# Kernel optimization log

Measured on AMD Instinct MI355X. Metric: run time of the kernel, lower is better.

Reference implementation:

```python
import jax, jax.numpy as jnp
import numpy as np

EPS = 1e-12  # torch F.normalize default eps


def conv1x1(x, w, b):
    # x: [N,C,H,W], w: [O,C], b: [O]
    return jnp.einsum('nchw,oc->nohw', x, w) + b[None, :, None, None]


def forward_sa(f1, f2, cw1, cb1, cw2, cb2):
    c1 = conv1x1(f1, cw1, cb1)  # [N,1,H,W]
    c2 = conv1x1(f2, cw2, cb2)
    n, _, h, w = c1.shape
    c1 = jax.nn.softmax(c1.reshape(n, 1, h * w), axis=-1).reshape(n, 1, h, w)
    c2 = jax.nn.softmax(c2.reshape(n, 1, h * w), axis=-1).reshape(n, 1, h, w)
    return c1 * f1, c2 * f2


def l2_normalize_ch(x):
    # F.normalize(x): L2 over channel dim (dim=1), norm clamped to eps
    n = jnp.sqrt(jnp.sum(x * x, axis=1, keepdims=True))
    return x / jnp.maximum(n, EPS)


def forward_ca(f1, f2, pw1, pb1, pw2, pb2):
    N, C, H, W = f1.shape
    HW = H * W
    f1_cl = conv1x1(f1, pw1, pb1).reshape(N, -1, HW)  # [N,Cl,HW]
    f2_cl = conv1x1(f2, pw2, pb2).reshape(N, -1, HW)
    # A = f2_cl^T @ f1_cl : [N,HW,HW]
    A_c = jnp.tanh(jnp.einsum('nci,ncj->nij', f2_cl, f1_cl))
    f1_v = f1.reshape(N, C, HW)
    f2_v = f2.reshape(N, C, HW)
    # f1_hat = f1_v @ A_c^T ; f2_hat = f2_v @ A_c
    f1_hat = jnp.einsum('ncj,nij->nci', f1_v, A_c).reshape(N, C, H, W)
    f2_hat = jnp.einsum('ncj,nji->nci', f2_v, A_c).reshape(N, C, H, W)
    return l2_normalize_ch(f1_hat), l2_normalize_ch(f2_hat)


def setup_inputs() -> dict:
    key = jax.random.key(0)
    ks = jax.random.split(key, 10)
    N, C, H, W = 8, 256, 32, 32
    Cl = C // 16
    return {
        'f1': jax.random.normal(ks[0], (N, C, H, W), jnp.float32),
        'f2': jax.random.normal(ks[1], (N, C, H, W), jnp.float32),
        'pw1': jax.random.normal(ks[2], (Cl, C), jnp.float32) * 0.05,
        'pb1': jax.random.normal(ks[3], (Cl,), jnp.float32) * 0.05,
        'pw2': jax.random.normal(ks[4], (Cl, C), jnp.float32) * 0.05,
        'pb2': jax.random.normal(ks[5], (Cl,), jnp.float32) * 0.05,
        'cw1': jax.random.normal(ks[6], (1, C), jnp.float32) * 0.05,
        'cb1': jax.random.normal(ks[7], (1,), jnp.float32) * 0.05,
        'cw2': jax.random.normal(ks[8], (1, C), jnp.float32) * 0.05,
        'cb2': jax.random.normal(ks[9], (1,), jnp.float32) * 0.05,
    }


def reference(f1, f2, pw1, pb1, pw2, pb2, cw1, cb1, cw2, cb2):
    fp1, fp2 = f1, f2
    for i in range(5):
        s1, s2 = forward_sa(fp1, fp2, cw1, cb1, cw2, cb2)
        h1, h2 = forward_ca(s1, s2, pw1, pb1, pw2, pb2)
        if i < 4:
            fp1 = jax.nn.relu(h1 + fp1)
            fp2 = jax.nn.relu(h2 + fp2)
    return h1, h2, s1, s2
```

## Files before the change

### kernel.cpp

```cpp
#include <hip/hip_runtime.h>
#include <cstdint>
#include <cstddef>

#define N_  8
#define C_  256
#define HW_ 1024
#define CL_ 16
#define SZ_ (N_*C_*HW_)
#define WSCALE_ 4096.0f

typedef __attribute__((ext_vector_type(8))) _Float16 half8;
typedef __attribute__((ext_vector_type(4))) float f32x4;

static __device__ __forceinline__ float tanh_fast(float x){
  x = fminf(fmaxf(x, -15.f), 15.f);
  float e = __expf(2.f * x);
  return (e - 1.f) / (e + 1.f);
}

static __device__ __forceinline__ unsigned short f2h(float x){
  _Float16 h = (_Float16)x;
  return *(unsigned short*)&h;
}

static __device__ __forceinline__ void combine16(
    const float* __restrict__ mpart, const float* __restrict__ spart,
    int base, float& m, float& rl)
{
  m = -1e30f;
  #pragma unroll
  for (int k = 0; k < 16; ++k) m = fmaxf(m, mpart[base * 16 + k]);
  float s = 0.f;
  #pragma unroll
  for (int k = 0; k < 16; ++k) s += spart[base * 16 + k] * __expf(mpart[base * 16 + k] - m);
  rl = 1.f / s;
}

#define GLD16(g, l) __builtin_amdgcn_global_load_lds( \
    (const __attribute__((address_space(1))) void*)(g), \
    (__attribute__((address_space(3))) void*)(l), 16, 0, 0)

__global__ __launch_bounds__(256) void k_cvt(
    const float* __restrict__ f1, const float* __restrict__ f2,
    _Float16* __restrict__ o1, _Float16* __restrict__ o2)
{
  const int side = blockIdx.y;
  const size_t o = ((size_t)blockIdx.x * 256 + threadIdx.x) * 8;
  const float* __restrict__ f = side ? f2 : f1;
  _Float16* __restrict__ oo = side ? o2 : o1;
  const float4 v0 = *(const float4*)&f[o];
  const float4 v1 = *(const float4*)&f[o + 4];
  half8 r;
  r[0] = (_Float16)v0.x; r[1] = (_Float16)v0.y; r[2] = (_Float16)v0.z; r[3] = (_Float16)v0.w;
  r[4] = (_Float16)v1.x; r[5] = (_Float16)v1.y; r[6] = (_Float16)v1.z; r[7] = (_Float16)v1.w;
  *(half8*)&oo[o] = r;
}

__global__ __launch_bounds__(256) void k_sa_dot(
    const float* __restrict__ fp1, const float* __restrict__ fp2,
    const float* __restrict__ cw1, const float* __restrict__ cw2,
    const float* __restrict__ pw1, const float* __restrict__ pw2,
    float* __restrict__ cval, float* __restrict__ pdot,
    float* __restrict__ mpart, float* __restrict__ spart)
{
  const int n = blockIdx.z, side = blockIdx.y, hw0 = blockIdx.x * 64;
  const int t = threadIdx.x, hwl = t & 63, cg = t >> 6;
  const float* __restrict__ pw = side ? pw2 : pw1;
  const float* __restrict__ cw = side ? cw2 : cw1;
  const float* __restrict__ f  = (side ? fp2 : fp1) + (size_t)n * C_ * HW_ + hw0 + hwl;
  const int cb = __builtin_amdgcn_readfirstlane(cg * 64);

  float acc[17];
  #pragma unroll
  for (int l = 0; l < 17; ++l) acc[l] = 0.f;

  for (int cc = 0; cc < 64; ++cc){
    const int c = cb + cc;
    const float v = f[(size_t)c * HW_];
    acc[16] += v * cw[c];
    #pragma unroll
    for (int l = 0; l < 16; ++l) acc[l] += v * pw[l * C_ + c];
  }

  __shared__ float red[17][4][64];
  #pragma unroll
  for (int l = 0; l < 17; ++l) red[l][cg][hwl] = acc[l];
  __syncthreads();

  if (t < 64){
    const int base = n * 2 + side;
    float xc = 0.f;
    #pragma unroll
    for (int l = 0; l < 17; ++l){
      const float s = red[l][0][t] + red[l][1][t] + red[l][2][t] + red[l][3][t];
      if (l < 16) pdot[((size_t)base * CL_ + l) * HW_ + hw0 + t] = s;
      else      { cval[(size_t)base * HW_ + hw0 + t] = s; xc = s; }
    }
    float mb = xc;
    #pragma unroll
    for (int off = 32; off; off >>= 1) mb = fmaxf(mb, __shfl_xor(mb, off));
    float e = __expf(xc - mb);
    #pragma unroll
    for (int off = 32; off; off >>= 1) e += __shfl_xor(e, off);
    if (t == 0){
      mpart[base * 16 + blockIdx.x] = mb;
      spart[base * 16 + blockIdx.x] = e;
    }
  }
}

__global__ __launch_bounds__(256) void k_corr(
    const float* __restrict__ cval, const float* __restrict__ pdot,
    const float* __restrict__ pb1, const float* __restrict__ pb2,
    const float* __restrict__ mpart, const float* __restrict__ spart,
    unsigned short* __restrict__ Abf, unsigned short* __restrict__ Atbf)
{
  const int n = blockIdx.z, i0 = blockIdx.y * 64, j0 = blockIdx.x * 64;
  const int b1 = n * 2, b2 = n * 2 + 1;
  __align__(16) __shared__ float s2[CL_][64];
  __align__(16) __shared__ float s1[CL_][64];
  __shared__ unsigned short at_s[64][68];
  const int t = threadIdx.x;
  const int lr = t >> 4, lc = (t & 15) * 4;

  float m1, rl1, m2, rl2;
  combine16(mpart, spart, b1, m1, rl1);
  combine16(mpart, spart, b2, m2, rl2);

  {
    const float bias2 = pb2[lr];
    const float4 c2 = *(const float4*)&cval[(size_t)b2 * HW_ + i0 + lc];
    const float4 p2 = *(const float4*)&pdot[((size_t)b2 * CL_ + lr) * HW_ + i0 + lc];
    s2[lr][lc + 0] = __expf(c2.x - m2) * rl2 * p2.x + bias2;
    s2[lr][lc + 1] = __expf(c2.y - m2) * rl2 * p2.y + bias2;
    s2[lr][lc + 2] = __expf(c2.z - m2) * rl2 * p2.z + bias2;
    s2[lr][lc + 3] = __expf(c2.w - m2) * rl2 * p2.w + bias2;

    const float bias1 = pb1[lr];
    const float4 c1 = *(const float4*)&cval[(size_t)b1 * HW_ + j0 + lc];
    const float4 p1 = *(const float4*)&pdot[((size_t)b1 * CL_ + lr) * HW_ + j0 + lc];
    s1[lr][lc + 0] = __expf(c1.x - m1) * rl1 * p1.x + bias1;
    s1[lr][lc + 1] = __expf(c1.y - m1) * rl1 * p1.y + bias1;
    s1[lr][lc + 2] = __expf(c1.z - m1) * rl1 * p1.z + bias1;
    s1[lr][lc + 3] = __expf(c1.w - m1) * rl1 * p1.w + bias1;
  }
  __syncthreads();

  const int ti = t >> 4, tj = t & 15;
  float acc[4][4];
  #pragma unroll
  for (int a = 0; a < 4; ++a)
    #pragma unroll
    for (int b = 0; b < 4; ++b) acc[a][b] = 0.f;

  #pragma unroll
  for (int l = 0; l < CL_; ++l){
    const float4 a4 = *(const float4*)&s2[l][ti * 4];
    const float4 b4 = *(const float4*)&s1[l][tj * 4];
    const float av[4] = {a4.x, a4.y, a4.z, a4.w};
    const float bv[4] = {b4.x, b4.y, b4.z, b4.w};
    #pragma unroll
    for (int a = 0; a < 4; ++a)
      #pragma unroll
      for (int b = 0; b < 4; ++b) acc[a][b] += av[a] * bv[b];
  }

  float tf[4][4];
  #pragma unroll
  for (int a = 0; a < 4; ++a)
    #pragma unroll
    for (int b = 0; b < 4; ++b) tf[a][b] = tanh_fast(acc[a][b]);

  float w1j[4], w2i[4];
  #pragma unroll
  for (int b = 0; b < 4; ++b)
    w1j[b] = WSCALE_ * __expf(cval[(size_t)b1 * HW_ + j0 + tj * 4 + b] - m1) * rl1;
  #pragma unroll
  for (int a = 0; a < 4; ++a)
    w2i[a] = WSCALE_ * __expf(cval[(size_t)b2 * HW_ + i0 + ti * 4 + a] - m2) * rl2;

  unsigned short* __restrict__ An  = Abf  + ((size_t)n << 20);
  unsigned short* __restrict__ Atn = Atbf + ((size_t)n << 20);
  #pragma unroll
  for (int a = 0; a < 4; ++a){
    ushort4 va;
    va.x = f2h(tf[a][0] * w1j[0]); va.y = f2h(tf[a][1] * w1j[1]);
    va.z = f2h(tf[a][2] * w1j[2]); va.w = f2h(tf[a][3] * w1j[3]);
    *(ushort4*)&An[(size_t)(i0 + ti * 4 + a) * HW_ + j0 + tj * 4] = va;
  }
  #pragma unroll
  for (int b = 0; b < 4; ++b){
    ushort4 vb;
    vb.x = f2h(tf[0][b] * w2i[0]); vb.y = f2h(tf[1][b] * w2i[1]);
    vb.z = f2h(tf[2][b] * w2i[2]); vb.w = f2h(tf[3][b] * w2i[3]);
    *(ushort4*)&at_s[tj * 4 + b][ti * 4] = vb;
  }
  __syncthreads();
  #pragma unroll
  for (int rep = 0; rep < 2; ++rep){
    const int idx = t + rep * 256;
    const int r = idx >> 3, q = (idx & 7) * 8;
    const ushort4 lo = *(const ushort4*)&at_s[r][q];
    const ushort4 hi = *(const ushort4*)&at_s[r][q + 4];
    *(ushort4*)&Atn[(size_t)(j0 + r) * HW_ + i0 + q] = lo;
    *(ushort4*)&Atn[(size_t)(j0 + r) * HW_ + i0 + q + 4] = hi;
  }
}

__global__ __launch_bounds__(512, 2) void k_gemm_fused(
    const _Float16* __restrict__ fhc1, const _Float16* __restrict__ fhc2,
    const unsigned short* __restrict__ Abf, const unsigned short* __restrict__ Atbf,
    const float* __restrict__ fpin1, const float* __restrict__ fpin2,
    float* __restrict__ fpo1, float* __restrict__ fpo2,
    _Float16* __restrict__ fhn1, _Float16* __restrict__ fhn2,
    const float* __restrict__ pw1, const float* __restrict__ pw2,
    const float* __restrict__ cw1, const float* __restrict__ cw2,
    float* __restrict__ cval, float* __restrict__ pdot,
    float* __restrict__ mpart, float* __restrict__ spart,
    float* __restrict__ out, int last)
{
  const int n = blockIdx.z, g = blockIdx.y, i0 = blockIdx.x * 64;
  const unsigned short* __restrict__ X =
      (const unsigned short*)((g ? fhc2 : fhc1) + (size_t)n * C_ * HW_);
  const unsigned short* __restrict__ B = (g ? Atbf : Abf) + ((size_t)n << 20);

  __shared__ __align__(16) unsigned char pool[81920];

  const int t = threadIdx.x, w = t >> 6, l = t & 63;
  const int wr = w >> 1, wc = w & 1;

  f32x4 acc[4][2];
  #pragma unroll
  for (int fm = 0; fm < 4; ++fm)
    #pragma unroll
    for (int fn = 0; fn < 2; ++fn)
      acc[fm][fn] = (f32x4){0.f, 0.f, 0.f, 0.f};

  auto stage = [&](int buf, int k0){
    unsigned short* Xsb = (unsigned short*)(pool + buf * 32768);
    unsigned short* Bsb = (unsigned short*)(pool + 65536 + buf * 8192);
    #pragma unroll
    for (int s = 0; s < 4; ++s){
      const int q = (w * 4 + s) * 64 + l;
      const int row = q >> 3;
      const int kc = (q & 7) ^ (row & 7);
      GLD16(X + (size_t)row * HW_ + k0 + kc * 8, &Xsb[(w * 4 + s) * 512]);
    }
    {
      const int q = w * 64 + l;
      const int row = q >> 3;
      const int kc = (q & 7) ^ (row & 7);
      GLD16(B + (size_t)(i0 + row) * HW_ + k0 + kc * 8, &Bsb[w * 512]);
    }
  };

  stage(0, 0);
  stage(1, 64);
  for (int kt = 0; kt < 16; ++kt){
    if (kt < 15) { asm volatile("s_waitcnt vmcnt(5)" ::: "memory"); }
    else         { asm volatile("s_waitcnt vmcnt(0)" ::: "memory"); }
    __builtin_amdgcn_sched_barrier(0);
    __builtin_amdgcn_s_barrier();
    const int cur = kt & 1;
    const unsigned short* Xsb = (const unsigned short*)(pool + cur * 32768);
    const unsigned short* Bsb = (const unsigned short*)(pool + 65536 + cur * 8192);
    #pragma unroll
    for (int ks = 0; ks < 2; ++ks){
      half8 a[4], bb[2];
      #pragma unroll
      for (int fm = 0; fm < 4; ++fm){
        const int row = wr * 64 + fm * 16 + (l & 15);
        const int kc = (ks * 4 + (l >> 4)) ^ (row & 7);
        a[fm] = *(const half8*)&Xsb[row * 64 + kc * 8];
      }
      #pragma unroll
      for (int fn = 0; fn < 2; ++fn){
        const int row = wc * 32 + fn * 16 + (l & 15);
        const int kc = (ks * 4 + (l >> 4)) ^ (row & 7);
        bb[fn] = *(const half8*)&Bsb[row * 64 + kc * 8];
      }
      #pragma unroll
      for (int fm = 0; fm < 4; ++fm)
        #pragma unroll
        for (int fn = 0; fn < 2; ++fn)
          acc[fm][fn] = __builtin_amdgcn_mfma_f32_16x16x32_f16(a[fm], bb[fn], acc[fm][fn], 0, 0, 0);
    }
    asm volatile("s_waitcnt lgkmcnt(0)" ::: "memory");
    __builtin_amdgcn_sched_barrier(0);
    __builtin_amdgcn_s_barrier();
    __builtin_amdgcn_sched_barrier(0);
    if (kt < 14) stage(cur, (kt + 2) * 64);
  }

  float* pwT   = (float*)pool;
  float* redp  = (float*)(pool + 32768);
  float* ssred = (float*)(pool + 65536);
  float* rinvp = (float*)(pool + 66560);

  float ss0 = 0.f, ss1 = 0.f;
  #pragma unroll
  for (int fm = 0; fm < 4; ++fm)
    #pragma unroll
    for (int r = 0; r < 4; ++r){
      ss0 += acc[fm][0][r] * acc[fm][0][r];
      ss1 += acc[fm][1][r] * acc[fm][1][r];
    }
  ss0 += __shfl_xor(ss0, 16); ss0 += __shfl_xor(ss0, 32);
  ss1 += __shfl_xor(ss1, 16); ss1 += __shfl_xor(ss1, 32);
  if (l < 16){
    ssred[wr * 64 + wc * 32 + l]      = ss0;
    ssred[wr * 64 + wc * 32 + 16 + l] = ss1;
  }

  if (!last){
    const float* __restrict__ pw = g ? pw2 : pw1;
    const float* __restrict__ cw = g ? cw2 : cw1;
    {
      const int idx = t * 8;
      const int lq = idx >> 8, c = idx & 255;
      const float4 p0 = *(const float4*)&pw[lq * C_ + c];
      const float4 p1 = *(const float4*)&pw[lq * C_ + c + 4];
      pwT[(c + 0) * 20 + lq] = p0.x; pwT[(c + 1) * 20 + lq] = p0.y;
      pwT[(c + 2) * 20 + lq] = p0.z; pwT[(c + 3) * 20 + lq] = p0.w;
      pwT[(c + 4) * 20 + lq] = p1.x; pwT[(c + 5) * 20 + lq] = p1.y;
      pwT[(c + 6) * 20 + lq] = p1.z; pwT[(c + 7) * 20 + lq] = p1.w;
    }
    if (t < 32){
      const float4 c0 = *(const float4*)&cw[t * 8];
      const float4 c1 = *(const float4*)&cw[t * 8 + 4];
      pwT[(t * 8 + 0) * 20 + 16] = c0.x; pwT[(t * 8 + 1) * 20 + 16] = c0.y;
      pwT[(t * 8 + 2) * 20 + 16] = c0.z; pwT[(t * 8 + 3) * 20 + 16] = c0.w;
      pwT[(t * 8 + 4) * 20 + 16] = c1.x; pwT[(t * 8 + 5) * 20 + 16] = c1.y;
      pwT[(t * 8 + 6) * 20 + 16] = c1.z; pwT[(t * 8 + 7) * 20 + 16] = c1.w;
    }
  }
  __syncthreads();
  if (t < 64){
    const float s = ssred[t] + ssred[64 + t] + ssred[128 + t] + ssred[192 + t];
    rinvp[t] = 1.f / fmaxf(sqrtf(s), 1e-12f);
  }
  __syncthreads();
  const float ri[2] = { rinvp[wc * 32 + (l & 15)], rinvp[wc * 32 + 16 + (l & 15)] };

  const float* __restrict__ fpin = (g ? fpin2 : fpin1) + (size_t)n * C_ * HW_;
  float* __restrict__ fpo  = (g ? fpo2 : fpo1) + (size_t)n * C_ * HW_;
  _Float16* __restrict__ fhn = (g ? fhn2 : fhn1) + (size_t)n * C_ * HW_;
  float* __restrict__ outp = out + (size_t)g * SZ_ + (size_t)n * C_ * HW_;
  const int rbase = (l >> 4) * 4, col = l & 15;
  const int baseio = n * 2 + g;

  if (!last){
    float sacc[2][17];
    #pragma unroll
    for (int fn = 0; fn < 2; ++fn)
      #pragma unroll
      for (int lq = 0; lq < 17; ++lq) sacc[fn][lq] = 0.f;

    #pragma unroll
    for (int fm = 0; fm < 4; ++fm)
      #pragma unroll
      for (int r = 0; r < 4; ++r){
        const int c = wr * 64 + fm * 16 + rbase + r;
        float prow[17];
        #pragma unroll
        for (int q4 = 0; q4 < 4; ++q4){
          const float4 pv = *(const float4*)&pwT[c * 20 + q4 * 4];
          prow[q4 * 4 + 0] = pv.x; prow[q4 * 4 + 1] = pv.y;
          prow[q4 * 4 + 2] = pv.z; prow[q4 * 4 + 3] = pv.w;
        }
        prow[16] = pwT[c * 20 + 16];
        #pragma unroll
        for (int fn = 0; fn < 2; ++fn){
          const size_t base = (size_t)c * HW_ + i0 + wc * 32 + fn * 16 + col;
          const float h = acc[fm][fn][r] * ri[fn];
          const float fv = fpin[base] + h;
          const float rv = fv > 0.f ? fv : 0.f;
          fpo[base] = rv;
          fhn[base] = (_Float16)rv;
          #pragma unroll
          for (int lq = 0; lq < 17; ++lq) sacc[fn][lq] += rv * prow[lq];
        }
      }

    #pragma unroll
    for (int fn = 0; fn < 2; ++fn)
      #pragma unroll
      for (int lq = 0; lq < 17; ++lq){
        float v = sacc[fn][lq];
        v += __shfl_xor(v, 16);
        v += __shfl_xor(v, 32);
        sacc[fn][lq] = v;
      }
    if (l < 16){
      #pragma unroll
      for (int fn = 0; fn < 2; ++fn)
        #pragma unroll
        for (int lq = 0; lq < 17; ++lq)
          redp[(((wr * 2 + wc) * 2 + fn) * 17 + lq) * 16 + l] = sacc[fn][lq];
    }
    __syncthreads();
    if (t < 64){
      const int wcx = t >> 5, fnx = (t >> 4) & 1, colx = t & 15;
      float xc = 0.f;
      #pragma unroll
      for (int lq = 0; lq < 17; ++lq){
        float s = 0.f;
        #pragma unroll
        for (int wrx = 0; wrx < 4; ++wrx)
          s += redp[(((wrx * 2 + wcx) * 2 + fnx) * 17 + lq) * 16 + colx];
        if (lq < 16) pdot[((size_t)baseio * CL_ + lq) * HW_ + i0 + t] = s;
        else       { cval[(size_t)baseio * HW_ + i0 + t] = s; xc = s; }
      }
      float mb = xc;
      #pragma unroll
      for (int off = 32; off; off >>= 1) mb = fmaxf(mb, __shfl_xor(mb, off));
      float e = __expf(xc - mb);
      #pragma unroll
      for (int off = 32; off; off >>= 1) e += __shfl_xor(e, off);
      if (t == 0){
        mpart[baseio * 16 + (i0 >> 6)] = mb;
        spart[baseio * 16 + (i0 >> 6)] = e;
      }
    }
  } else {
    #pragma unroll
    for (int fm = 0; fm < 4; ++fm)
      #pragma unroll
      for (int fn = 0; fn < 2; ++fn){
        const size_t base = (size_t)(wr * 64 + fm * 16 + rbase) * HW_ + i0 + wc * 32 + fn * 16 + col;
        #pragma unroll
        for (int r = 0; r < 4; ++r)
          outp[base + (size_t)r * HW_] = acc[fm][fn][r] * ri[fn];
      }
  }
}

__global__ __launch_bounds__(256) void k_s_out(
    const float* __restrict__ fp1, const float* __restrict__ fp2,
    const float* __restrict__ cval,
    const float* __restrict__ mpart, const float* __restrict__ spart,
    float* __restrict__ out)
{
  const int side = blockIdx.y;
  const size_t fo = ((size_t)blockIdx.x * 256 + threadIdx.x) * 4;
  const float* __restrict__ f = side ? fp2 : fp1;
  const int n  = (int)(fo >> 18);
  const int hw = (int)(fo & (HW_ - 1));
  const int base = n * 2 + side;
  float m, rl;
  combine16(mpart, spart, base, m, rl);
  const float4 c = *(const float4*)&cval[(size_t)base * HW_ + hw];
  const float4 v = *(const float4*)&f[fo];
  float4 r;
  r.x = v.x * (__expf(c.x - m) * rl);
  r.y = v.y * (__expf(c.y - m) * rl);
  r.z = v.z * (__expf(c.z - m) * rl);
  r.w = v.w * (__expf(c.w - m) * rl);
  *(float4*)&out[(size_t)(2 + side) * SZ_ + fo] = r;
}

extern "C" void kernel_launch(void* const* d_in, const int* in_sizes, int n_in,
                              void* d_out, int out_size, void* d_ws, size_t ws_size,
                              hipStream_t stream)
{
  const float* f1  = (const float*)d_in[0];
  const float* f2  = (const float*)d_in[1];
  const float* pw1 = (const float*)d_in[2];
  const float* pb1 = (const float*)d_in[3];
  const float* pw2 = (const float*)d_in[4];
  const float* pb2 = (const float*)d_in[5];
  const float* cw1 = (const float*)d_in[6];
  const float* cw2 = (const float*)d_in[8];
  float* out = (float*)d_out;
  float* ws  = (float*)d_ws;

  float* cval  = ws;
  float* pdot  = cval + N_ * 2 * HW_;
  float* mpart = pdot + N_ * 2 * CL_ * HW_;
  float* spart = mpart + 512;
  float* fp1   = spart + 512;
  float* fp2   = fp1 + SZ_;
  _Float16* fhA1 = (_Float16*)(fp2 + SZ_);
  _Float16* fhA2 = fhA1 + SZ_;
  _Float16* fhB1 = fhA2 + SZ_;
  _Float16* fhB2 = fhB1 + SZ_;
  unsigned short* Abf  = (unsigned short*)(fhB2 + SZ_);
  unsigned short* Atbf = Abf + ((size_t)N_ << 20);

  k_cvt<<<dim3(SZ_ / 8 / 256, 2), 256, 0, stream>>>(f1, f2, fhA1, fhA2);
  k_sa_dot<<<dim3(16, 2, 8), 256, 0, stream>>>(f1, f2, cw1, cw2, pw1, pw2,
                                               cval, pdot, mpart, spart);

  for (int it = 0; it < 5; ++it){
    const float* cur1 = (it == 0) ? f1 : fp1;
    const float* cur2 = (it == 0) ? f2 : fp2;
    const _Float16* fhc1 = (it & 1) ? fhB1 : fhA1;
    const _Float16* fhc2 = (it & 1) ? fhB2 : fhA2;
    _Float16* fhn1 = (it & 1) ? fhA1 : fhB1;
    _Float16* fhn2 = (it & 1) ? fhA2 : fhB2;

    k_corr<<<dim3(16, 16, 8), 256, 0, stream>>>(cval, pdot, pb1, pb2, mpart, spart, Abf, Atbf);
    if (it == 4)
      k_s_out<<<dim3(SZ_ / 4 / 256, 2), 256, 0, stream>>>(cur1, cur2, cval, mpart, spart, out);
    k_gemm_fused<<<dim3(16, 2, 8), 512, 0, stream>>>(fhc1, fhc2, Abf, Atbf,
                                                     cur1, cur2, fp1, fp2, fhn1, fhn2,
                                                     pw1, pw2, cw1, cw2,
                                                     cval, pdot, mpart, spart,
                                                     out, (it == 4) ? 1 : 0);
  }
}
```

Measured before the change: 243.1 us.

## Fuse correlation matrix computation into GEMM kernel flash-style, drop A materialization

Removes the separate k_corr kernel that wrote the tanh-weighted HW×HW correlation matrix and its transpose to global memory. The matrix tiles are now recomputed on the fly inside the main GEMM kernel with MFMA, using split fp16 hi/lo operands to keep precision, and overlapped with the double-buffered X loads. The fp16 conversion is also folded into k_sa_dot, and the s-output write into the last GEMM iteration, removing two more launches. In exchange, each of the two side blocks recomputes the tiles redundantly, and the kernel uses more shared memory, which may lower occupancy.

```diff
diff --git a/kernel.cpp b/kernel.cpp
--- a/kernel.cpp
+++ b/kernel.cpp
@@ -40,34 +40,20 @@
     (const __attribute__((address_space(1))) void*)(g), \
     (__attribute__((address_space(3))) void*)(l), 16, 0, 0)
 
-__global__ __launch_bounds__(256) void k_cvt(
-    const float* __restrict__ f1, const float* __restrict__ f2,
-    _Float16* __restrict__ o1, _Float16* __restrict__ o2)
-{
-  const int side = blockIdx.y;
-  const size_t o = ((size_t)blockIdx.x * 256 + threadIdx.x) * 8;
-  const float* __restrict__ f = side ? f2 : f1;
-  _Float16* __restrict__ oo = side ? o2 : o1;
-  const float4 v0 = *(const float4*)&f[o];
-  const float4 v1 = *(const float4*)&f[o + 4];
-  half8 r;
-  r[0] = (_Float16)v0.x; r[1] = (_Float16)v0.y; r[2] = (_Float16)v0.z; r[3] = (_Float16)v0.w;
-  r[4] = (_Float16)v1.x; r[5] = (_Float16)v1.y; r[6] = (_Float16)v1.z; r[7] = (_Float16)v1.w;
-  *(half8*)&oo[o] = r;
-}
-
 __global__ __launch_bounds__(256) void k_sa_dot(
     const float* __restrict__ fp1, const float* __restrict__ fp2,
     const float* __restrict__ cw1, const float* __restrict__ cw2,
     const float* __restrict__ pw1, const float* __restrict__ pw2,
     float* __restrict__ cval, float* __restrict__ pdot,
-    float* __restrict__ mpart, float* __restrict__ spart)
+    float* __restrict__ mpart, float* __restrict__ spart,
+    _Float16* __restrict__ fh1, _Float16* __restrict__ fh2)
 {
   const int n = blockIdx.z, side = blockIdx.y, hw0 = blockIdx.x * 64;
   const int t = threadIdx.x, hwl = t & 63, cg = t >> 6;
   const float* __restrict__ pw = side ? pw2 : pw1;
   const float* __restrict__ cw = side ? cw2 : cw1;
   const float* __restrict__ f  = (side ? fp2 : fp1) + (size_t)n * C_ * HW_ + hw0 + hwl;
+  _Float16* __restrict__ fh = (side ? fh2 : fh1) + (size_t)n * C_ * HW_ + hw0 + hwl;
   const int cb = __builtin_amdgcn_readfirstlane(cg * 64);
 
   float acc[17];
@@ -77,6 +63,7 @@
   for (int cc = 0; cc < 64; ++cc){
     const int c = cb + cc;
     const float v = f[(size_t)c * HW_];
+    fh[(size_t)c * HW_] = (_Float16)v;
     acc[16] += v * cw[c];
     #pragma unroll
     for (int l = 0; l < 16; ++l) acc[l] += v * pw[l * C_ + c];
@@ -109,112 +96,14 @@
   }
 }
 
-__global__ __launch_bounds__(256) void k_corr(
-    const float* __restrict__ cval, const float* __restrict__ pdot,
-    const float* __restrict__ pb1, const float* __restrict__ pb2,
-    const float* __restrict__ mpart, const float* __restrict__ spart,
-    unsigned short* __restrict__ Abf, unsigned short* __restrict__ Atbf)
-{
-  const int n = blockIdx.z, i0 = blockIdx.y * 64, j0 = blockIdx.x * 64;
-  const int b1 = n * 2, b2 = n * 2 + 1;
-  __align__(16) __shared__ float s2[CL_][64];
-  __align__(16) __shared__ float s1[CL_][64];
-  __shared__ unsigned short at_s[64][68];
-  const int t = threadIdx.x;
-  const int lr = t >> 4, lc = (t & 15) * 4;
-
-  float m1, rl1, m2, rl2;
-  combine16(mpart, spart, b1, m1, rl1);
-  combine16(mpart, spart, b2, m2, rl2);
-
-  {
-    const float bias2 = pb2[lr];
-    const float4 c2 = *(const float4*)&cval[(size_t)b2 * HW_ + i0 + lc];
-    const float4 p2 = *(const float4*)&pdot[((size_t)b2 * CL_ + lr) * HW_ + i0 + lc];
-    s2[lr][lc + 0] = __expf(c2.x - m2) * rl2 * p2.x + bias2;
-    s2[lr][lc + 1] = __expf(c2.y - m2) * rl2 * p2.y + bias2;
-    s2[lr][lc + 2] = __expf(c2.z - m2) * rl2 * p2.z + bias2;
-    s2[lr][lc + 3] = __expf(c2.w - m2) * rl2 * p2.w + bias2;
-
-    const float bias1 = pb1[lr];
-    const float4 c1 = *(const float4*)&cval[(size_t)b1 * HW_ + j0 + lc];
-    const float4 p1 = *(const float4*)&pdot[((size_t)b1 * CL_ + lr) * HW_ + j0 + lc];
-    s1[lr][lc + 0] = __expf(c1.x - m1) * rl1 * p1.x + bias1;
-    s1[lr][lc + 1] = __expf(c1.y - m1) * rl1 * p1.y + bias1;
-    s1[lr][lc + 2] = __expf(c1.z - m1) * rl1 * p1.z + bias1;
-    s1[lr][lc + 3] = __expf(c1.w - m1) * rl1 * p1.w + bias1;
-  }
-  __syncthreads();
-
-  const int ti = t >> 4, tj = t & 15;
-  float acc[4][4];
-  #pragma unroll
-  for (int a = 0; a < 4; ++a)
-    #pragma unroll
-    for (int b = 0; b < 4; ++b) acc[a][b] = 0.f;
-
-  #pragma unroll
-  for (int l = 0; l < CL_; ++l){
-    const float4 a4 = *(const float4*)&s2[l][ti * 4];
-    const float4 b4 = *(const float4*)&s1[l][tj * 4];
-    const float av[4] = {a4.x, a4.y, a4.z, a4.w};
-    const float bv[4] = {b4.x, b4.y, b4.z, b4.w};
-    #pragma unroll
-    for (int a = 0; a < 4; ++a)
-      #pragma unroll
-      for (int b = 0; b < 4; ++b) acc[a][b] += av[a] * bv[b];
-  }
-
-  float tf[4][4];
-  #pragma unroll
-  for (int a = 0; a < 4; ++a)
-    #pragma unroll
-    for (int b = 0; b < 4; ++b) tf[a][b] = tanh_fast(acc[a][b]);
-
-  float w1j[4], w2i[4];
-  #pragma unroll
-  for (int b = 0; b < 4; ++b)
-    w1j[b] = WSCALE_ * __expf(cval[(size_t)b1 * HW_ + j0 + tj * 4 + b] - m1) * rl1;
-  #pragma unroll
-  for (int a = 0; a < 4; ++a)
-    w2i[a] = WSCALE_ * __expf(cval[(size_t)b2 * HW_ + i0 + ti * 4 + a] - m2) * rl2;
-
-  unsigned short* __restrict__ An  = Abf  + ((size_t)n << 20);
-  unsigned short* __restrict__ Atn = Atbf + ((size_t)n << 20);
-  #pragma unroll
-  for (int a = 0; a < 4; ++a){
-    ushort4 va;
-    va.x = f2h(tf[a][0] * w1j[0]); va.y = f2h(tf[a][1] * w1j[1]);
-    va.z = f2h(tf[a][2] * w1j[2]); va.w = f2h(tf[a][3] * w1j[3]);
-    *(ushort4*)&An[(size_t)(i0 + ti * 4 + a) * HW_ + j0 + tj * 4] = va;
-  }
-  #pragma unroll
-  for (int b = 0; b < 4; ++b){
-    ushort4 vb;
-    vb.x = f2h(tf[0][b] * w2i[0]); vb.y = f2h(tf[1][b] * w2i[1]);
-    vb.z = f2h(tf[2][b] * w2i[2]); vb.w = f2h(tf[3][b] * w2i[3]);
-    *(ushort4*)&at_s[tj * 4 + b][ti * 4] = vb;
-  }
-  __syncthreads();
-  #pragma unroll
-  for (int rep = 0; rep < 2; ++rep){
-    const int idx = t + rep * 256;
-    const int r = idx >> 3, q = (idx & 7) * 8;
-    const ushort4 lo = *(const ushort4*)&at_s[r][q];
-    const ushort4 hi = *(const ushort4*)&at_s[r][q + 4];
-    *(ushort4*)&Atn[(size_t)(j0 + r) * HW_ + i0 + q] = lo;
-    *(ushort4*)&Atn[(size_t)(j0 + r) * HW_ + i0 + q + 4] = hi;
-  }
-}
-
-__global__ __launch_bounds__(512, 2) void k_gemm_fused(
+__global__ __launch_bounds__(512, 2) void k_flash(
     const _Float16* __restrict__ fhc1, const _Float16* __restrict__ fhc2,
-    const unsigned short* __restrict__ Abf, const unsigned short* __restrict__ Atbf,
     const float* __restrict__ fpin1, const float* __restrict__ fpin2,
     float* __restrict__ fpo1, float* __restrict__ fpo2,
     _Float16* __restrict__ fhn1, _Float16* __restrict__ fhn2,
     const float* __restrict__ pw1, const float* __restrict__ pw2,
     const float* __restrict__ cw1, const float* __restrict__ cw2,
+    const float* __restrict__ pb1, const float* __restrict__ pb2,
     float* __restrict__ cval, float* __restrict__ pdot,
     float* __restrict__ mpart, float* __restrict__ spart,
     float* __restrict__ out, int last)
@@ -222,9 +111,28 @@
   const int n = blockIdx.z, g = blockIdx.y, i0 = blockIdx.x * 64;
   const unsigned short* __restrict__ X =
       (const unsigned short*)((g ? fhc2 : fhc1) + (size_t)n * C_ * HW_);
-  const unsigned short* __restrict__ B = (g ? Atbf : Abf) + ((size_t)n << 20);
-
-  __shared__ __align__(16) unsigned char pool[81920];
+
+  const int baseP = n * 2 + 1 - g;
+  const int baseQ = n * 2 + g;
+  const float* __restrict__ pbP = g ? pb1 : pb2;
+  const float* __restrict__ pbQ = g ? pb2 : pb1;
+  const float* __restrict__ cvalP = cval + (size_t)baseP * HW_;
+  const float* __restrict__ cvalQ = cval + (size_t)baseQ * HW_;
+  const float* __restrict__ pdotP = pdot + (size_t)baseP * CL_ * HW_;
+  const float* __restrict__ pdotQ = pdot + (size_t)baseQ * CL_ * HW_;
+
+  float mP, rlP, mQ, rlQ;
+  combine16(mpart, spart, baseP, mP, rlP);
+  combine16(mpart, spart, baseQ, mQ, rlQ);
+
+  __shared__ __align__(16) unsigned char pool[118784];
+  #define XSP(buf) ((unsigned short*)(pool + (buf) * 32768))
+  #define BSP(buf) ((unsigned short*)(pool + 65536 + (buf) * 8192))
+  #define QTA(qb)  ((_Float16*)(pool + 81920 + (qb) * 15360))
+  #define QTB(qb)  ((_Float16*)(pool + 81920 + (qb) * 15360 + 5120))
+  #define QTC(qb)  ((_Float16*)(pool + 81920 + (qb) * 15360 + 10240))
+  #define PTH      ((_Float16*)(pool + 112640))
+  #define WQSP(qb) ((float*)(pool + 117760 + (qb) * 256))
 
   const int t = threadIdx.x, w = t >> 6, l = t & 63;
   const int wr = w >> 1, wc = w & 1;
@@ -237,8 +145,7 @@
       acc[fm][fn] = (f32x4){0.f, 0.f, 0.f, 0.f};
 
   auto stage = [&](int buf, int k0){
-    unsigned short* Xsb = (unsigned short*)(pool + buf * 32768);
-    unsigned short* Bsb = (unsigned short*)(pool + 65536 + buf * 8192);
+    unsigned short* Xsb = XSP(buf);
     #pragma unroll
     for (int s = 0; s < 4; ++s){
       const int q = (w * 4 + s) * 64 + l;
@@ -246,24 +153,93 @@
       const int kc = (q & 7) ^ (row & 7);
       GLD16(X + (size_t)row * HW_ + k0 + kc * 8, &Xsb[(w * 4 + s) * 512]);
     }
-    {
-      const int q = w * 64 + l;
-      const int row = q >> 3;
-      const int kc = (q & 7) ^ (row & 7);
-      GLD16(B + (size_t)(i0 + row) * HW_ + k0 + kc * 8, &Bsb[w * 512]);
-    }
   };
 
+  auto q_build = [&](int jt){
+    const int qb = jt & 1;
+    const int col = t & 63, lg = t >> 6;
+    const int j = jt * 64 + col;
+    const float wq = __expf(cvalQ[j] - mQ) * rlQ;
+    if (lg == 0) WQSP(qb)[col] = WSCALE_ * wq;
+    #pragma unroll
+    for (int u = 0; u < 2; ++u){
+      const int lq = lg * 2 + u;
+      const float q = wq * pdotQ[(size_t)lq * HW_ + j] + pbQ[lq];
+      const _Float16 qh = (_Float16)q;
+      const _Float16 ql = (_Float16)((q - (float)qh) * 256.0f);
+      QTA(qb)[col * 40 + lq] = qh;
+      QTB(qb)[col * 40 + 16 + lq] = qh;
+      QTC(qb)[col * 40 + lq] = ql;
+    }
+  };
+
+  auto s_build = [&](int jt, int bw){
+    const int qb = jt & 1;
+    const _Float16* qa = QTA(qb); const _Float16* qbb = QTB(qb); const _Float16* qc = QTC(qb);
+    const float* wqp = WQSP(qb);
+    unsigned short* bs = BSP(bw);
+    #pragma unroll
+    for (int s2 = 0; s2 < 2; ++s2){
+      const int f = w * 2 + s2, si = f >> 2, sj = f & 3;
+      const int prow = si * 16 + (l & 15), qrow = sj * 16 + (l & 15);
+      const half8 ap = *(const half8*)&PTH[prow * 40 + (l >> 4) * 8];
+      const half8 bA = *(const half8*)&qa [qrow * 40 + (l >> 4) * 8];
+      const half8 bB = *(const half8*)&qbb[qrow * 40 + (l >> 4) * 8];
+      const half8 bC = *(const half8*)&qc [qrow * 40 + (l >> 4) * 8];
+      const f32x4 z = (f32x4){0.f, 0.f, 0.f, 0.f};
+      const f32x4 d1 = __builtin_amdgcn_mfma_f32_16x16x32_f16(ap, bA, z, 0, 0, 0);
+      const f32x4 d2 = __builtin_amdgcn_mfma_f32_16x16x32_f16(ap, bB, z, 0, 0, 0);
+      const f32x4 d3 = __builtin_amdgcn_mfma_f32_16x16x32_f16(ap, bC, z, 0, 0, 0);
+      const float wqv = wqp[qrow];
+      #pragma unroll
+      for (int r = 0; r < 4; ++r){
+        const float S = d1[r] + 0.00390625f * (d2[r] + d3[r]);
+        const int irow = si * 16 + (l >> 4) * 4 + r;
+        bs[irow * 64 + (((qrow >> 3) ^ (irow & 7)) * 8) + (qrow & 7)]
+            = f2h(tanh_fast(S) * wqv);
+      }
+    }
+  };
+
+  {
+    uint4* z = (uint4*)(pool + 81920);
+    for (int idx = t; idx < 2272; idx += 512) z[idx] = (uint4){0, 0, 0, 0};
+  }
+  __syncthreads();
   stage(0, 0);
   stage(1, 64);
+  {
+    const int col = t & 63, lg = t >> 6;
+    const float wp = __expf(cvalP[i0 + col] - mP) * rlP;
+    #pragma unroll
+    for (int u = 0; u < 2; ++u){
+      const int lq = lg * 2 + u;
+      const float p = wp * pdotP[(size_t)lq * HW_ + i0 + col] + pbP[lq];
+      const _Float16 ph = (_Float16)p;
+      const _Float16 pl = (_Float16)((p - (float)ph) * 256.0f);
+      PTH[col * 40 + lq] = ph;
+      PTH[col * 40 + 16 + lq] = pl;
+    }
+  }
+  q_build(0);
+  asm volatile("s_waitcnt lgkmcnt(0)" ::: "memory");
+  __builtin_amdgcn_sched_barrier(0);
+  __builtin_amdgcn_s_barrier();
+  s_build(0, 0);
+  q_build(1);
+  asm volatile("s_waitcnt lgkmcnt(0)" ::: "memory");
+  __builtin_amdgcn_sched_barrier(0);
+  __builtin_amdgcn_s_barrier();
+
+  int cur = 0;
   for (int kt = 0; kt < 16; ++kt){
-    if (kt < 15) { asm volatile("s_waitcnt vmcnt(5)" ::: "memory"); }
-    else         { asm volatile("s_waitcnt vmcnt(0)" ::: "memory"); }
+    if (kt < 15) { asm volatile("s_waitcnt vmcnt(4) lgkmcnt(0)" ::: "memory"); }
+    else         { asm volatile("s_waitcnt vmcnt(0) lgkmcnt(0)" ::: "memory"); }
     __builtin_amdgcn_sched_barrier(0);
     __builtin_amdgcn_s_barrier();
-    const int cur = kt & 1;
-    const unsigned short* Xsb = (const unsigned short*)(pool + cur * 32768);
-    const unsigned short* Bsb = (const unsigned short*)(pool + 65536 + cur * 8192);
+
+    const unsigned short* Xsb = XSP(cur);
+    const unsigned short* Bsb = BSP(cur);
     #pragma unroll
     for (int ks = 0; ks < 2; ++ks){
       half8 a[4], bb[2];
@@ -285,11 +261,18 @@
         for (int fn = 0; fn < 2; ++fn)
           acc[fm][fn] = __builtin_amdgcn_mfma_f32_16x16x32_f16(a[fm], bb[fn], acc[fm][fn], 0, 0, 0);
     }
+    if (kt < 15) s_build(kt + 1, cur ^ 1);
+
     asm volatile("s_waitcnt lgkmcnt(0)" ::: "memory");
     __builtin_amdgcn_sched_barrier(0);
     __builtin_amdgcn_s_barrier();
     __builtin_amdgcn_sched_barrier(0);
-    if (kt < 14) stage(cur, (kt + 2) * 64);
+
+    if (kt < 14){
+      q_build(kt + 2);
+      stage(cur, (kt + 2) * 64);
+    }
+    cur ^= 1;
   }
 
   float* pwT   = (float*)pool;
@@ -423,40 +406,30 @@
       }
     }
   } else {
+    float* __restrict__ out2p = out + (size_t)(2 + g) * SZ_ + (size_t)n * C_ * HW_;
+    float wv[2];
+    #pragma unroll
+    for (int fn = 0; fn < 2; ++fn)
+      wv[fn] = __expf(cvalQ[i0 + wc * 32 + fn * 16 + col] - mQ) * rlQ;
     #pragma unroll
     for (int fm = 0; fm < 4; ++fm)
       #pragma unroll
       for (int fn = 0; fn < 2; ++fn){
         const size_t base = (size_t)(wr * 64 + fm * 16 + rbase) * HW_ + i0 + wc * 32 + fn * 16 + col;
         #pragma unroll
-        for (int r = 0; r < 4; ++r)
+        for (int r = 0; r < 4; ++r){
           outp[base + (size_t)r * HW_] = acc[fm][fn][r] * ri[fn];
-      }
-  }
-}
-
-__global__ __launch_bounds__(256) void k_s_out(
-    const float* __restrict__ fp1, const float* __restrict__ fp2,
-    const float* __restrict__ cval,
-    const float* __restrict__ mpart, const float* __restrict__ spart,
-    float* __restrict__ out)
-{
-  const int side = blockIdx.y;
-  const size_t fo = ((size_t)blockIdx.x * 256 + threadIdx.x) * 4;
-  const float* __restrict__ f = side ? fp2 : fp1;
-  const int n  = (int)(fo >> 18);
-  const int hw = (int)(fo & (HW_ - 1));
-  const int base = n * 2 + side;
-  float m, rl;
-  combine16(mpart, spart, base, m, rl);
-  const float4 c = *(const float4*)&cval[(size_t)base * HW_ + hw];
-  const float4 v = *(const float4*)&f[fo];
-  float4 r;
-  r.x = v.x * (__expf(c.x - m) * rl);
-  r.y = v.y * (__expf(c.y - m) * rl);
-  r.z = v.z * (__expf(c.z - m) * rl);
-  r.w = v.w * (__expf(c.w - m) * rl);
-  *(float4*)&out[(size_t)(2 + side) * SZ_ + fo] = r;
+          out2p[base + (size_t)r * HW_] = wv[fn] * fpin[base + (size_t)r * HW_];
+        }
+      }
+  }
+  #undef XSP
+  #undef BSP
+  #undef QTA
+  #undef QTB
+  #undef QTC
+  #undef PTH
+  #undef WQSP
 }
 
 extern "C" void kernel_launch(void* const* d_in, const int* in_sizes, int n_in,
@@ -484,12 +457,9 @@
   _Float16* fhA2 = fhA1 + SZ_;
   _Float16* fhB1 = fhA2 + SZ_;
   _Float16* fhB2 = fhB1 + SZ_;
-  unsigned short* Abf  = (unsigned short*)(fhB2 + SZ_);
-  unsigned short* Atbf = Abf + ((size_t)N_ << 20);
-
-  k_cvt<<<dim3(SZ_ / 8 / 256, 2), 256, 0, stream>>>(f1, f2, fhA1, fhA2);
+
   k_sa_dot<<<dim3(16, 2, 8), 256, 0, stream>>>(f1, f2, cw1, cw2, pw1, pw2,
-                                               cval, pdot, mpart, spart);
+                                               cval, pdot, mpart, spart, fhA1, fhA2);
 
   for (int it = 0; it < 5; ++it){
     const float* cur1 = (it == 0) ? f1 : fp1;
@@ -499,13 +469,10 @@
     _Float16* fhn1 = (it & 1) ? fhA1 : fhB1;
     _Float16* fhn2 = (it & 1) ? fhA2 : fhB2;
 
-    k_corr<<<dim3(16, 16, 8), 256, 0, stream>>>(cval, pdot, pb1, pb2, mpart, spart, Abf, Atbf);
-    if (it == 4)
-      k_s_out<<<dim3(SZ_ / 4 / 256, 2), 256, 0, stream>>>(cur1, cur2, cval, mpart, spart, out);
-    k_gemm_fused<<<dim3(16, 2, 8), 512, 0, stream>>>(fhc1, fhc2, Abf, Atbf,
-                                                     cur1, cur2, fp1, fp2, fhn1, fhn2,
-                                                     pw1, pw2, cw1, cw2,
-                                                     cval, pdot, mpart, spart,
-                                                     out, (it == 4) ? 1 : 0);
-  }
-}
+    k_flash<<<dim3(16, 2, 8), 512, 0, stream>>>(fhc1, fhc2,
+                                                cur1, cur2, fp1, fp2, fhn1, fhn2,
+                                                pw1, pw2, cw1, cw2, pb1, pb2,
+                                                cval, pdot, mpart, spart,
+                                                out, (it == 4) ? 1 : 0);
+  }
+}
```

After: 244.1 us. Within noise of the previous version (+0.4%).

## Halve GEMM column tile to double grid; fuse fp16 conversion into sa_dot

Applied to the files above, without the earlier changes.

The fused GEMM kernel now computes 32 output columns per block instead of 64, doubling the grid from 256 to 512 blocks and shrinking LDS use so more blocks can reside per CU. The softmax partials are reorganised into 32 chunks per row to match the new tile width. The separate fp32-to-fp16 conversion kernel is removed, and k_sa_dot writes the fp16 copy as it reads the input. In exchange, each block reloads the full X operand for half as much output, which doubles X traffic through L2, and the MFMA work per LDS load drops.

```diff
diff --git a/kernel.cpp b/kernel.cpp
--- a/kernel.cpp
+++ b/kernel.cpp
@@ -23,51 +23,37 @@
   return *(unsigned short*)&h;
 }
 
-static __device__ __forceinline__ void combine16(
+static __device__ __forceinline__ void combine32(
     const float* __restrict__ mpart, const float* __restrict__ spart,
     int base, float& m, float& rl)
 {
   m = -1e30f;
   #pragma unroll
-  for (int k = 0; k < 16; ++k) m = fmaxf(m, mpart[base * 16 + k]);
+  for (int k = 0; k < 32; ++k) m = fmaxf(m, mpart[base * 32 + k]);
   float s = 0.f;
   #pragma unroll
-  for (int k = 0; k < 16; ++k) s += spart[base * 16 + k] * __expf(mpart[base * 16 + k] - m);
+  for (int k = 0; k < 32; ++k) s += spart[base * 32 + k] * __expf(mpart[base * 32 + k] - m);
   rl = 1.f / s;
 }
 
 #define GLD16(g, l) __builtin_amdgcn_global_load_lds( \
     (const __attribute__((address_space(1))) void*)(g), \
     (__attribute__((address_space(3))) void*)(l), 16, 0, 0)
-
-__global__ __launch_bounds__(256) void k_cvt(
-    const float* __restrict__ f1, const float* __restrict__ f2,
-    _Float16* __restrict__ o1, _Float16* __restrict__ o2)
-{
-  const int side = blockIdx.y;
-  const size_t o = ((size_t)blockIdx.x * 256 + threadIdx.x) * 8;
-  const float* __restrict__ f = side ? f2 : f1;
-  _Float16* __restrict__ oo = side ? o2 : o1;
-  const float4 v0 = *(const float4*)&f[o];
-  const float4 v1 = *(const float4*)&f[o + 4];
-  half8 r;
-  r[0] = (_Float16)v0.x; r[1] = (_Float16)v0.y; r[2] = (_Float16)v0.z; r[3] = (_Float16)v0.w;
-  r[4] = (_Float16)v1.x; r[5] = (_Float16)v1.y; r[6] = (_Float16)v1.z; r[7] = (_Float16)v1.w;
-  *(half8*)&oo[o] = r;
-}
 
 __global__ __launch_bounds__(256) void k_sa_dot(
     const float* __restrict__ fp1, const float* __restrict__ fp2,
     const float* __restrict__ cw1, const float* __restrict__ cw2,
     const float* __restrict__ pw1, const float* __restrict__ pw2,
     float* __restrict__ cval, float* __restrict__ pdot,
-    float* __restrict__ mpart, float* __restrict__ spart)
+    float* __restrict__ mpart, float* __restrict__ spart,
+    _Float16* __restrict__ fh1, _Float16* __restrict__ fh2)
 {
   const int n = blockIdx.z, side = blockIdx.y, hw0 = blockIdx.x * 64;
   const int t = threadIdx.x, hwl = t & 63, cg = t >> 6;
   const float* __restrict__ pw = side ? pw2 : pw1;
   const float* __restrict__ cw = side ? cw2 : cw1;
   const float* __restrict__ f  = (side ? fp2 : fp1) + (size_t)n * C_ * HW_ + hw0 + hwl;
+  _Float16* __restrict__ fh = (side ? fh2 : fh1) + (size_t)n * C_ * HW_ + hw0 + hwl;
   const int cb = __builtin_amdgcn_readfirstlane(cg * 64);
 
   float acc[17];
@@ -77,6 +63,7 @@
   for (int cc = 0; cc < 64; ++cc){
     const int c = cb + cc;
     const float v = f[(size_t)c * HW_];
+    fh[(size_t)c * HW_] = (_Float16)v;
     acc[16] += v * cw[c];
     #pragma unroll
     for (int l = 0; l < 16; ++l) acc[l] += v * pw[l * C_ + c];
@@ -98,13 +85,13 @@
     }
     float mb = xc;
     #pragma unroll
-    for (int off = 32; off; off >>= 1) mb = fmaxf(mb, __shfl_xor(mb, off));
+    for (int off = 16; off; off >>= 1) mb = fmaxf(mb, __shfl_xor(mb, off));
     float e = __expf(xc - mb);
     #pragma unroll
-    for (int off = 32; off; off >>= 1) e += __shfl_xor(e, off);
-    if (t == 0){
-      mpart[base * 16 + blockIdx.x] = mb;
-      spart[base * 16 + blockIdx.x] = e;
+    for (int off = 16; off; off >>= 1) e += __shfl_xor(e, off);
+    if (t == 0 || t == 32){
+      mpart[base * 32 + (hw0 >> 5) + (t >> 5)] = mb;
+      spart[base * 32 + (hw0 >> 5) + (t >> 5)] = e;
     }
   }
 }
@@ -124,8 +111,8 @@
   const int lr = t >> 4, lc = (t & 15) * 4;
 
   float m1, rl1, m2, rl2;
-  combine16(mpart, spart, b1, m1, rl1);
-  combine16(mpart, spart, b2, m2, rl2);
+  combine32(mpart, spart, b1, m1, rl1);
+  combine32(mpart, spart, b2, m2, rl2);
 
   {
     const float bias2 = pb2[lr];
@@ -207,7 +194,7 @@
   }
 }
 
-__global__ __launch_bounds__(512, 2) void k_gemm_fused(
+__global__ __launch_bounds__(512, 4) void k_gemm_fused(
     const _Float16* __restrict__ fhc1, const _Float16* __restrict__ fhc2,
     const unsigned short* __restrict__ Abf, const unsigned short* __restrict__ Atbf,
     const float* __restrict__ fpin1, const float* __restrict__ fpin2,
@@ -219,26 +206,22 @@
     float* __restrict__ mpart, float* __restrict__ spart,
     float* __restrict__ out, int last)
 {
-  const int n = blockIdx.z, g = blockIdx.y, i0 = blockIdx.x * 64;
+  const int n = blockIdx.z, g = blockIdx.y, i0 = blockIdx.x * 32;
   const unsigned short* __restrict__ X =
       (const unsigned short*)((g ? fhc2 : fhc1) + (size_t)n * C_ * HW_);
   const unsigned short* __restrict__ B = (g ? Atbf : Abf) + ((size_t)n << 20);
 
-  __shared__ __align__(16) unsigned char pool[81920];
+  __shared__ __align__(16) unsigned char pool[73728];
 
   const int t = threadIdx.x, w = t >> 6, l = t & 63;
   const int wr = w >> 1, wc = w & 1;
 
-  f32x4 acc[4][2];
-  #pragma unroll
-  for (int fm = 0; fm < 4; ++fm)
-    #pragma unroll
-    for (int fn = 0; fn < 2; ++fn)
-      acc[fm][fn] = (f32x4){0.f, 0.f, 0.f, 0.f};
+  f32x4 acc[4];
+  #pragma unroll
+  for (int fm = 0; fm < 4; ++fm) acc[fm] = (f32x4){0.f, 0.f, 0.f, 0.f};
 
   auto stage = [&](int buf, int k0){
     unsigned short* Xsb = (unsigned short*)(pool + buf * 32768);
-    unsigned short* Bsb = (unsigned short*)(pool + 65536 + buf * 8192);
     #pragma unroll
     for (int s = 0; s < 4; ++s){
       const int q = (w * 4 + s) * 64 + l;
@@ -246,7 +229,8 @@
       const int kc = (q & 7) ^ (row & 7);
       GLD16(X + (size_t)row * HW_ + k0 + kc * 8, &Xsb[(w * 4 + s) * 512]);
     }
-    {
+    if (w < 4){
+      unsigned short* Bsb = (unsigned short*)(pool + 65536 + buf * 4096);
       const int q = w * 64 + l;
       const int row = q >> 3;
       const int kc = (q & 7) ^ (row & 7);
@@ -257,33 +241,32 @@
   stage(0, 0);
   stage(1, 64);
   for (int kt = 0; kt < 16; ++kt){
-    if (kt < 15) { asm volatile("s_waitcnt vmcnt(5)" ::: "memory"); }
-    else         { asm volatile("s_waitcnt vmcnt(0)" ::: "memory"); }
+    if (kt < 15){
+      if (w < 4) { asm volatile("s_waitcnt vmcnt(5)" ::: "memory"); }
+      else       { asm volatile("s_waitcnt vmcnt(4)" ::: "memory"); }
+    } else       { asm volatile("s_waitcnt vmcnt(0)" ::: "memory"); }
     __builtin_amdgcn_sched_barrier(0);
     __builtin_amdgcn_s_barrier();
     const int cur = kt & 1;
     const unsigned short* Xsb = (const unsigned short*)(pool + cur * 32768);
-    const unsigned short* Bsb = (const unsigned short*)(pool + 65536 + cur * 8192);
+    const unsigned short* Bsb = (const unsigned short*)(pool + 65536 + cur * 4096);
     #pragma unroll
     for (int ks = 0; ks < 2; ++ks){
-      half8 a[4], bb[2];
+      half8 a[4], bb;
       #pragma unroll
       for (int fm = 0; fm < 4; ++fm){
         const int row = wr * 64 + fm * 16 + (l & 15);
         const int kc = (ks * 4 + (l >> 4)) ^ (row & 7);
         a[fm] = *(const half8*)&Xsb[row * 64 + kc * 8];
       }
-      #pragma unroll
-      for (int fn = 0; fn < 2; ++fn){
-        const int row = wc * 32 + fn * 16 + (l & 15);
+      {
+        const int row = wc * 16 + (l & 15);
         const int kc = (ks * 4 + (l >> 4)) ^ (row & 7);
-        bb[fn] = *(const half8*)&Bsb[row * 64 + kc * 8];
+        bb = *(const half8*)&Bsb[row * 64 + kc * 8];
       }
       #pragma unroll
       for (int fm = 0; fm < 4; ++fm)
-        #pragma unroll
-        for (int fn = 0; fn < 2; ++fn)
-          acc[fm][fn] = __builtin_amdgcn_mfma_f32_16x16x32_f16(a[fm], bb[fn], acc[fm][fn], 0, 0, 0);
+        acc[fm] = __builtin_amdgcn_mfma_f32_16x16x32_f16(a[fm], bb, acc[fm], 0, 0, 0);
     }
     asm volatile("s_waitcnt lgkmcnt(0)" ::: "memory");
     __builtin_amdgcn_sched_barrier(0);
@@ -297,20 +280,14 @@
   float* ssred = (float*)(pool + 65536);
   float* rinvp = (float*)(pool + 66560);
 
-  float ss0 = 0.f, ss1 = 0.f;
+  float ss = 0.f;
   #pragma unroll
   for (int fm = 0; fm < 4; ++fm)
     #pragma unroll
-    for (int r = 0; r < 4; ++r){
-      ss0 += acc[fm][0][r] * acc[fm][0][r];
-      ss1 += acc[fm][1][r] * acc[fm][1][r];
-    }
-  ss0 += __shfl_xor(ss0, 16); ss0 += __shfl_xor(ss0, 32);
-  ss1 += __shfl_xor(ss1, 16); ss1 += __shfl_xor(ss1, 32);
-  if (l < 16){
-    ssred[wr * 64 + wc * 32 + l]      = ss0;
-    ssred[wr * 64 + wc * 32 + 16 + l] = ss1;
-  }
+    for (int r = 0; r < 4; ++r) ss += acc[fm][r] * acc[fm][r];
+  ss += __shfl_xor(ss, 16);
+  ss += __shfl_xor(ss, 32);
+  if (l < 16) ssred[wr * 32 + wc * 16 + l] = ss;
 
   if (!last){
     const float* __restrict__ pw = g ? pw2 : pw1;
@@ -335,12 +312,12 @@
     }
   }
   __syncthreads();
-  if (t < 64){
-    const float s = ssred[t] + ssred[64 + t] + ssred[128 + t] + ssred[192 + t];
+  if (t < 32){
+    const float s = ssred[t] + ssred[32 + t] + ssred[64 + t] + ssred[96 + t];
     rinvp[t] = 1.f / fmaxf(sqrtf(s), 1e-12f);
   }
   __syncthreads();
-  const float ri[2] = { rinvp[wc * 32 + (l & 15)], rinvp[wc * 32 + 16 + (l & 15)] };
+  const float ri = rinvp[wc * 16 + (l & 15)];
 
   const float* __restrict__ fpin = (g ? fpin2 : fpin1) + (size_t)n * C_ * HW_;
   float* __restrict__ fpo  = (g ? fpo2 : fpo1) + (size_t)n * C_ * HW_;
@@ -350,11 +327,9 @@
   const int baseio = n * 2 + g;
 
   if (!last){
-    float sacc[2][17];
-    #pragma unroll
-    for (int fn = 0; fn < 2; ++fn)
-      #pragma unroll
-      for (int lq = 0; lq < 17; ++lq) sacc[fn][lq] = 0.f;
+    float sacc[17];
+    #pragma unroll
+    for (int lq = 0; lq < 17; ++lq) sacc[lq] = 0.f;
 
     #pragma unroll
     for (int fm = 0; fm < 4; ++fm)
@@ -369,69 +344,60 @@
           prow[q4 * 4 + 2] = pv.z; prow[q4 * 4 + 3] = pv.w;
         }
         prow[16] = pwT[c * 20 + 16];
+        const size_t base = (size_t)c * HW_ + i0 + wc * 16 + col;
+        const float h = acc[fm][r] * ri;
+        const float fv = fpin[base] + h;
+        const float rv = fv > 0.f ? fv : 0.f;
+        fpo[base] = rv;
+        fhn[base] = (_Float16)rv;
         #pragma unroll
-        for (int fn = 0; fn < 2; ++fn){
-          const size_t base = (size_t)c * HW_ + i0 + wc * 32 + fn * 16 + col;
-          const float h = acc[fm][fn][r] * ri[fn];
-          const float fv = fpin[base] + h;
-          const float rv = fv > 0.f ? fv : 0.f;
-          fpo[base] = rv;
-          fhn[base] = (_Float16)rv;
-          #pragma unroll
-          for (int lq = 0; lq < 17; ++lq) sacc[fn][lq] += rv * prow[lq];
-        }
+        for (int lq = 0; lq < 17; ++lq) sacc[lq] += rv * prow[lq];
       }
 
     #pragma unroll
-    for (int fn = 0; fn < 2; ++fn)
-      #pragma unroll
-      for (int lq = 0; lq < 17; ++lq){
-        float v = sacc[fn][lq];
-        v += __shfl_xor(v, 16);
-        v += __shfl_xor(v, 32);
-        sacc[fn][lq] = v;
-      }
+    for (int lq = 0; lq < 17; ++lq){
+      float v = sacc[lq];
+      v += __shfl_xor(v, 16);
+      v += __shfl_xor(v, 32);
+      sacc[lq] = v;
+    }
     if (l < 16){
       #pragma unroll
-      for (int fn = 0; fn < 2; ++fn)
-        #pragma unroll
-        for (int lq = 0; lq < 17; ++lq)
-          redp[(((wr * 2 + wc) * 2 + fn) * 17 + lq) * 16 + l] = sacc[fn][lq];
+      for (int lq = 0; lq < 17; ++lq)
+        redp[((wr * 2 + wc) * 17 + lq) * 16 + l] = sacc[lq];
     }
     __syncthreads();
-    if (t < 64){
-      const int wcx = t >> 5, fnx = (t >> 4) & 1, colx = t & 15;
+    if (t < 32){
+      const int wcx = t >> 4, colx = t & 15;
       float xc = 0.f;
       #pragma unroll
       for (int lq = 0; lq < 17; ++lq){
         float s = 0.f;
         #pragma unroll
         for (int wrx = 0; wrx < 4; ++wrx)
-          s += redp[(((wrx * 2 + wcx) * 2 + fnx) * 17 + lq) * 16 + colx];
+          s += redp[((wrx * 2 + wcx) * 17 + lq) * 16 + colx];
         if (lq < 16) pdot[((size_t)baseio * CL_ + lq) * HW_ + i0 + t] = s;
         else       { cval[(size_t)baseio * HW_ + i0 + t] = s; xc = s; }
       }
       float mb = xc;
       #pragma unroll
-      for (int off = 32; off; off >>= 1) mb = fmaxf(mb, __shfl_xor(mb, off));
+      for (int off = 16; off; off >>= 1) mb = fmaxf(mb, __shfl_xor(mb, off));
       float e = __expf(xc - mb);
       #pragma unroll
-      for (int off = 32; off; off >>= 1) e += __shfl_xor(e, off);
+      for (int off = 16; off; off >>= 1) e += __shfl_xor(e, off);
       if (t == 0){
-        mpart[baseio * 16 + (i0 >> 6)] = mb;
-        spart[baseio * 16 + (i0 >> 6)] = e;
+        mpart[baseio * 32 + (i0 >> 5)] = mb;
+        spart[baseio * 32 + (i0 >> 5)] = e;
       }
     }
   } else {
     #pragma unroll
-    for (int fm = 0; fm < 4; ++fm)
-      #pragma unroll
-      for (int fn = 0; fn < 2; ++fn){
-        const size_t base = (size_t)(wr * 64 + fm * 16 + rbase) * HW_ + i0 + wc * 32 + fn * 16 + col;
-        #pragma unroll
-        for (int r = 0; r < 4; ++r)
-          outp[base + (size_t)r * HW_] = acc[fm][fn][r] * ri[fn];
-      }
+    for (int fm = 0; fm < 4; ++fm){
+      const size_t base = (size_t)(wr * 64 + fm * 16 + rbase) * HW_ + i0 + wc * 16 + col;
+      #pragma unroll
+      for (int r = 0; r < 4; ++r)
+        outp[base + (size_t)r * HW_] = acc[fm][r] * ri;
+    }
   }
 }
 
@@ -448,7 +414,7 @@
   const int hw = (int)(fo & (HW_ - 1));
   const int base = n * 2 + side;
   float m, rl;
-  combine16(mpart, spart, base, m, rl);
+  combine32(mpart, spart, base, m, rl);
   const float4 c = *(const float4*)&cval[(size_t)base * HW_ + hw];
   const float4 v = *(const float4*)&f[fo];
   float4 r;
@@ -487,9 +453,8 @@
   unsigned short* Abf  = (unsigned short*)(fhB2 + SZ_);
   unsigned short* Atbf = Abf + ((size_t)N_ << 20);
 
-  k_cvt<<<dim3(SZ_ / 8 / 256, 2), 256, 0, stream>>>(f1, f2, fhA1, fhA2);
   k_sa_dot<<<dim3(16, 2, 8), 256, 0, stream>>>(f1, f2, cw1, cw2, pw1, pw2,
-                                               cval, pdot, mpart, spart);
+                                               cval, pdot, mpart, spart, fhA1, fhA2);
 
   for (int it = 0; it < 5; ++it){
     const float* cur1 = (it == 0) ? f1 : fp1;
@@ -502,7 +467,7 @@
     k_corr<<<dim3(16, 16, 8), 256, 0, stream>>>(cval, pdot, pb1, pb2, mpart, spart, Abf, Atbf);
     if (it == 4)
       k_s_out<<<dim3(SZ_ / 4 / 256, 2), 256, 0, stream>>>(cur1, cur2, cval, mpart, spart, out);
-    k_gemm_fused<<<dim3(16, 2, 8), 512, 0, stream>>>(fhc1, fhc2, Abf, Atbf,
+    k_gemm_fused<<<dim3(32, 2, 8), 512, 0, stream>>>(fhc1, fhc2, Abf, Atbf,
                                                      cur1, cur2, fp1, fp2, fhn1, fhn2,
                                                      pw1, pw2, cw1, cw2,
                                                      cval, pdot, mpart, spart,
```

After: 272.4 us. +12.0%, slower.
